# Kernel optimization log

Hardware: AMD Instinct MI355X
Metric: run time of the kernel (lower is better)

The kernel has to match this reference:

```python
import jax, jax.numpy as jnp
from jax import lax
import numpy as np

BETA = 0.9
SLOPE = 25.0  # snntorch fast_sigmoid default slope

@jax.custom_vjp
def spike_fn(mem_shift):
    # Heaviside forward, fast-sigmoid surrogate backward
    return (mem_shift > 0).astype(mem_shift.dtype)

def _spike_fwd(mem_shift):
    return spike_fn(mem_shift), mem_shift

def _spike_bwd(mem_shift, g):
    return (g / (SLOPE * jnp.abs(mem_shift) + 1.0) ** 2,)

spike_fn.defvjp(_spike_fwd, _spike_bwd)

def lif_step(inp, mem, thr):
    # snntorch Leaky, reset_mechanism='subtract': reset computed from PREVIOUS mem, detached
    reset = lax.stop_gradient((mem - thr > 0).astype(mem.dtype))
    mem_new = BETA * mem + inp - reset * thr  # thr keeps grad through reset term
    spk = spike_fn(mem_new - thr)
    return spk, mem_new

def _linear_init(key, out_f, in_f):
    k1, k2 = jax.random.split(key)
    bound = 1.0 / np.sqrt(in_f)
    W = jax.random.uniform(k1, (out_f, in_f), jnp.float32, -bound, bound)
    b = jax.random.uniform(k2, (out_f,), jnp.float32, -bound, bound)
    return W, b

def setup_inputs() -> dict:
    key = jax.random.key(0)
    ks = jax.random.split(key, 6)
    B, T = 2048, 112
    x = jax.random.normal(ks[0], (B, T, 4), jnp.float32)
    W1, b1 = _linear_init(ks[1], 1300, 4)
    W2, b2 = _linear_init(ks[2], 340, 1300)
    W3, b3 = _linear_init(ks[3], 1400, 340)
    W4, b4 = _linear_init(ks[4], 4, 1400)
    return {
        'x': x,
        'W1': W1, 'b1': b1, 'bias1': jnp.zeros((1300,), jnp.float32),
        'W2': W2, 'b2': b2, 'bias2': jnp.zeros((340,), jnp.float32),
        'W3': W3, 'b3': b3, 'bias3': jnp.zeros((1400,), jnp.float32),
        'W4': W4, 'b4': b4, 'bias4': jnp.zeros((4,), jnp.float32),
        'thr4': jnp.asarray(0.5, jnp.float32),
    }

def reference(x, W1, b1, bias1, W2, b2, bias2, W3, b3, bias3, W4, b4, bias4, thr4):
    B, T, _ = x.shape
    one = jnp.asarray(1.0, x.dtype)

    def step(carry, xt):
        m1, m2, m3, m4 = carry
        xt = xt / 50.0 + 0.001
        s1, m1 = lif_step(xt @ W1.T + b1 + bias1, m1, one)
        s2, m2 = lif_step(s1 @ W2.T + b2 + bias2, m2, one)
        s3, m3 = lif_step(s2 @ W3.T + b3 + bias3, m3, one)
        s4, m4 = lif_step(s3 @ W4.T + b4 + bias4, m4, thr4)
        return (m1, m2, m3, m4), s4

    init = tuple(jnp.zeros((B, d), x.dtype) for d in (1300, 340, 1400, 4))
    _, spk4 = lax.scan(step, init, jnp.swapaxes(x, 0, 1))  # [T,B,4]
    spk4_stack = jnp.swapaxes(spk4, 0, 1)  # [B,T,4]
    spike_counts = spk4_stack.sum(axis=1)  # [B,4]
    return spike_counts, spk4_stack
```

## Files before the change

### kernel.cpp

```cpp
#include <hip/hip_runtime.h>

#define B_ROWS  2048
#define T_STEPS 112
#define N1 1300
#define N2 340
#define N3 1400

#define R1 192
#define R2 64
#define R3 192

#define OFF_W2T 0
#define OFF_W3T 442000
#define OFF_W4T 918000
#define OFF_BS1 923600
#define OFF_BS2 924900
#define OFF_BS3 925240
#define OFF_BS4 926640
#define WS_FLOATS 926644

__global__ __launch_bounds__(256) void snn_prep(
    const float* __restrict__ W2, const float* __restrict__ W3, const float* __restrict__ W4,
    const float* __restrict__ b1, const float* __restrict__ bias1,
    const float* __restrict__ b2, const float* __restrict__ bias2,
    const float* __restrict__ b3, const float* __restrict__ bias3,
    const float* __restrict__ b4, const float* __restrict__ bias4,
    float* __restrict__ ws)
{
    for (int idx = blockIdx.x * blockDim.x + threadIdx.x; idx < WS_FLOATS;
         idx += gridDim.x * blockDim.x) {
        float v;
        if (idx < OFF_W3T) {
            int j = idx; int i = j / N2, k = j % N2;
            v = W2[k * N1 + i];
        } else if (idx < OFF_W4T) {
            int j = idx - OFF_W3T; int i = j / N3, k = j % N3;
            v = W3[k * N2 + i];
        } else if (idx < OFF_BS1) {
            int j = idx - OFF_W4T; int i = j / 4, k = j % 4;
            v = W4[k * N3 + i];
        } else if (idx < OFF_BS2) { int j = idx - OFF_BS1; v = b1[j] + bias1[j]; }
        else if (idx < OFF_BS3)   { int j = idx - OFF_BS2; v = b2[j] + bias2[j]; }
        else if (idx < OFF_BS4)   { int j = idx - OFF_BS3; v = b3[j] + bias3[j]; }
        else                      { int j = idx - OFF_BS4; v = b4[j] + bias4[j]; }
        ws[idx] = v;
    }
}

__device__ __forceinline__ float2 pk_add(float2 a, float2 b) {
    float2 d;
    asm("v_pk_add_f32 %0, %1, %2" : "=v"(d) : "v"(a), "v"(b));
    return d;
}
__device__ __forceinline__ void pk_acc4(float4& acc, const float4 r) {
    float2 lo = pk_add(make_float2(acc.x, acc.y), make_float2(r.x, r.y));
    float2 hi = pk_add(make_float2(acc.z, acc.w), make_float2(r.z, r.w));
    acc.x = lo.x; acc.y = lo.y; acc.z = hi.x; acc.w = hi.y;
}

__global__ __launch_bounds__(512, 4) void snn_main(
    const float* __restrict__ x,
    const float* __restrict__ W1,
    const float* __restrict__ ws,
    const float* __restrict__ thr4p,
    float* __restrict__ out)
{
    const int b    = blockIdx.x;
    const int tid  = threadIdx.x;
    const int wave = tid >> 6;
    const int lane = tid & 63;

    const float* __restrict__ W2T = ws + OFF_W2T;
    const float* __restrict__ W3T = ws + OFF_W3T;
    const float* __restrict__ W4T = ws + OFF_W4T;
    const float* __restrict__ bs1 = ws + OFF_BS1;
    const float* __restrict__ bs2 = ws + OFF_BS2;
    const float* __restrict__ bs3 = ws + OFF_BS3;
    const float* __restrict__ bs4 = ws + OFF_BS4;

    __shared__ __align__(16) float pw2[8][340];
    __shared__ __align__(16) float pw3[8][1400];
    __shared__ __align__(16) unsigned short lst1[8 * R1];
    __shared__ __align__(16) unsigned short lst2[8 * R2];
    __shared__ __align__(16) unsigned short lst3[8 * R3];
    __shared__ float h4part[8][4];

    const int c1b = (wave < 5) ? 3 * wave : 15 + 2 * (wave - 5);
    const int n1  = (wave < 5) ? 3 : 2;

    float mem1[3] = {0.f,0.f,0.f};
    float mem2 = 0.f;
    float mem3[3] = {0.f,0.f,0.f};
    float mem4 = 0.f;
    float cnt  = 0.f;
    const float thr4 = thr4p[0];

    const float4* __restrict__ xv4 = (const float4*)x;
    const float4* __restrict__ W1v = (const float4*)W1;

    int  k1v[3]; bool val1[3]; float bsv1[3];
    #pragma unroll
    for (int u = 0; u < 3; ++u) {
        k1v[u] = (c1b + u) * 64 + lane;
        val1[u] = (u < n1) && (k1v[u] < N1);
        bsv1[u] = val1[u] ? bs1[k1v[u]] : 0.f;
    }
    const bool  act2 = (tid < N2);
    const float bs2v = act2 ? bs2[tid] : 0.f;
    const bool  act3hi = (tid < 376);
    float bs3v[3];
    bs3v[0] = bs3[tid];
    bs3v[1] = bs3[tid + 512];
    bs3v[2] = act3hi ? bs3[tid + 1024] : 0.f;
    const float bs4v = bs4[lane & 3];

    const int so2 = (lane < 21) ? 4 * lane : 80;
    const int so3 = (lane < 30) ? 4 * lane : 116;

    for (int t = 0; t < T_STEPS; ++t) {
        float4 xv = xv4[b * T_STEPS + t];
        const float x0 = xv.x / 50.0f + 0.001f;
        const float x1 = xv.y / 50.0f + 0.001f;
        const float x2 = xv.z / 50.0f + 0.001f;
        const float x3 = xv.w / 50.0f + 0.001f;

        unsigned cnt1w = 0;
        #pragma unroll
        for (int u = 0; u < 3; ++u) {
            if (u < n1) {
                float h = 0.f;
                if (val1[u]) {
                    float4 wv = W1v[k1v[u]];
                    h = bsv1[u] + wv.x * x0 + wv.y * x1 + wv.z * x2 + wv.w * x3;
                }
                float m = mem1[u];
                const float r = (m > 1.0f) ? 1.0f : 0.0f;
                m = 0.9f * m + h - r;
                mem1[u] = m;
                const bool sp = val1[u] && (m > 1.0f);
                const unsigned long long bal = __ballot(sp);
                if (sp) {
                    const int pos = (int)cnt1w + (int)__popcll(bal & ((1ull << lane) - 1ull));
                    lst1[wave * R1 + pos] = (unsigned short)k1v[u];
                }
                cnt1w += (unsigned)__popcll(bal);
            }
        }

        {
            float4 accA = {0.f,0.f,0.f,0.f};
            float4 accB = {0.f,0.f,0.f,0.f};
            const unsigned short* L = lst1 + wave * R1;
            const float* baseA = W2T + 4 * lane;
            const float* baseB = W2T + 256 + so2;
            const int n = (int)cnt1w;
            int j = 0;
            if (n >= 4) {
                ushort4 i0 = *(const ushort4*)(L);
                int o0 = (int)i0.x * N2, o1 = (int)i0.y * N2;
                int o2 = (int)i0.z * N2, o3 = (int)i0.w * N2;
                float4 rA0 = *(const float4*)(baseA + o0);
                float4 rA1 = *(const float4*)(baseA + o1);
                float4 rA2 = *(const float4*)(baseA + o2);
                float4 rA3 = *(const float4*)(baseA + o3);
                float4 rB0 = *(const float4*)(baseB + o0);
                float4 rB1 = *(const float4*)(baseB + o1);
                float4 rB2 = *(const float4*)(baseB + o2);
                float4 rB3 = *(const float4*)(baseB + o3);
                for (j = 4; j + 4 <= n; j += 4) {
                    ushort4 i1 = *(const ushort4*)(L + j);
                    const int p0 = (int)i1.x * N2, p1 = (int)i1.y * N2;
                    const int p2 = (int)i1.z * N2, p3 = (int)i1.w * N2;
                    float4 sA0 = *(const float4*)(baseA + p0);
                    float4 sA1 = *(const float4*)(baseA + p1);
                    float4 sA2 = *(const float4*)(baseA + p2);
                    float4 sA3 = *(const float4*)(baseA + p3);
                    float4 sB0 = *(const float4*)(baseB + p0);
                    float4 sB1 = *(const float4*)(baseB + p1);
                    float4 sB2 = *(const float4*)(baseB + p2);
                    float4 sB3 = *(const float4*)(baseB + p3);
                    pk_acc4(accA, rA0); pk_acc4(accB, rB0);
                    pk_acc4(accA, rA1); pk_acc4(accB, rB1);
                    pk_acc4(accA, rA2); pk_acc4(accB, rB2);
                    pk_acc4(accA, rA3); pk_acc4(accB, rB3);
                    rA0 = sA0; rA1 = sA1; rA2 = sA2; rA3 = sA3;
                    rB0 = sB0; rB1 = sB1; rB2 = sB2; rB3 = sB3;
                }
                pk_acc4(accA, rA0); pk_acc4(accB, rB0);
                pk_acc4(accA, rA1); pk_acc4(accB, rB1);
                pk_acc4(accA, rA2); pk_acc4(accB, rB2);
                pk_acc4(accA, rA3); pk_acc4(accB, rB3);
            }
            for (; j < n; ++j) {
                const int o = (int)L[j] * N2;
                float4 rA = *(const float4*)(baseA + o);
                float4 rB = *(const float4*)(baseB + o);
                pk_acc4(accA, rA); pk_acc4(accB, rB);
            }
            *(float4*)&pw2[wave][4 * lane] = accA;
            if (lane < 21) *(float4*)&pw2[wave][256 + 4 * lane] = accB;
        }
        __syncthreads();

        if (wave == 7 && t > 0) {
            float h4 = bs4v;
            #pragma unroll
            for (int p = 0; p < 8; ++p) h4 += h4part[p][lane & 3];
            float m4 = mem4;
            const float r4 = (m4 > thr4) ? thr4 : 0.f;
            m4 = 0.9f * m4 + h4 - r4;
            mem4 = m4;
            const float s4 = (m4 > thr4) ? 1.f : 0.f;
            if (lane < 4) {
                out[8192 + (b * T_STEPS + (t - 1)) * 4 + lane] = s4;
                cnt += s4;
            }
        }

        unsigned cnt2w = 0;
        {
            float h0 = 0.f;
            if (act2) {
                h0 = pw2[0][tid] + pw2[1][tid] + pw2[2][tid] + pw2[3][tid]
                   + pw2[4][tid] + pw2[5][tid] + pw2[6][tid] + pw2[7][tid] + bs2v;
            }
            float m = mem2;
            const float r = (m > 1.0f) ? 1.0f : 0.0f;
            m = 0.9f * m + h0 - r;
            mem2 = m;
            const bool sp0 = act2 && (m > 1.0f);
            const unsigned long long bal0 = __ballot(sp0);
            if (sp0) {
                const int pos = (int)__popcll(bal0 & ((1ull << lane) - 1ull));
                lst2[wave * R2 + pos] = (unsigned short)tid;
            }
            cnt2w = (unsigned)__popcll(bal0);
        }

        {
            float4 acc3[6];
            #pragma unroll
            for (int c = 0; c < 6; ++c) acc3[c] = (float4){0.f,0.f,0.f,0.f};
            const unsigned short* L = lst2 + wave * R2;
            int j = 0;
            for (; j + 2 <= (int)cnt2w; j += 2) {
                ushort2 ii = *(const ushort2*)(L + j);
                const float* ra = W3T + (int)ii.x * N3;
                const float* rb = W3T + (int)ii.y * N3;
                float4 a0 = *(const float4*)(ra + 4*lane);
                float4 a1 = *(const float4*)(ra + 256 + 4*lane);
                float4 a2 = *(const float4*)(ra + 512 + 4*lane);
                float4 a3 = *(const float4*)(ra + 768 + 4*lane);
                float4 a4 = *(const float4*)(ra + 1024 + 4*lane);
                float4 a5 = *(const float4*)(ra + 1280 + so3);
                float4 b0 = *(const float4*)(rb + 4*lane);
                float4 b1_ = *(const float4*)(rb + 256 + 4*lane);
                float4 b2_ = *(const float4*)(rb + 512 + 4*lane);
                float4 b3_ = *(const float4*)(rb + 768 + 4*lane);
                float4 b4_ = *(const float4*)(rb + 1024 + 4*lane);
                float4 b5_ = *(const float4*)(rb + 1280 + so3);
                pk_acc4(acc3[0], a0); pk_acc4(acc3[1], a1); pk_acc4(acc3[2], a2);
                pk_acc4(acc3[3], a3); pk_acc4(acc3[4], a4); pk_acc4(acc3[5], a5);
                pk_acc4(acc3[0], b0); pk_acc4(acc3[1], b1_); pk_acc4(acc3[2], b2_);
                pk_acc4(acc3[3], b3_); pk_acc4(acc3[4], b4_); pk_acc4(acc3[5], b5_);
            }
            for (; j < (int)cnt2w; ++j) {
                const float* ra = W3T + (int)L[j] * N3;
                float4 a0 = *(const float4*)(ra + 4*lane);
                float4 a1 = *(const float4*)(ra + 256 + 4*lane);
                float4 a2 = *(const float4*)(ra + 512 + 4*lane);
                float4 a3 = *(const float4*)(ra + 768 + 4*lane);
                float4 a4 = *(const float4*)(ra + 1024 + 4*lane);
                float4 a5 = *(const float4*)(ra + 1280 + so3);
                pk_acc4(acc3[0], a0); pk_acc4(acc3[1], a1); pk_acc4(acc3[2], a2);
                pk_acc4(acc3[3], a3); pk_acc4(acc3[4], a4); pk_acc4(acc3[5], a5);
            }
            #pragma unroll
            for (int c = 0; c < 5; ++c)
                *(float4*)&pw3[wave][c * 256 + 4 * lane] = acc3[c];
            if (lane < 30) *(float4*)&pw3[wave][1280 + 4 * lane] = acc3[5];
        }
        __syncthreads();

        {
            unsigned cnt3w = 0;
            #pragma unroll
            for (int k = 0; k < 3; ++k) {
                const bool valid = (k < 2) || act3hi;
                const int n = tid + 512 * k;
                float h = 0.f;
                if (valid) {
                    h = pw3[0][n] + pw3[1][n] + pw3[2][n] + pw3[3][n]
                      + pw3[4][n] + pw3[5][n] + pw3[6][n] + pw3[7][n] + bs3v[k];
                }
                float m = mem3[k];
                const float r = (m > 1.0f) ? 1.0f : 0.0f;
                m = 0.9f * m + h - r;
                mem3[k] = m;
                const bool sp = valid && (m > 1.0f);
                const unsigned long long bal = __ballot(sp);
                if (sp) {
                    const int pos = (int)cnt3w + (int)__popcll(bal & ((1ull << lane) - 1ull));
                    lst3[wave * R3 + pos] = (unsigned short)n;
                }
                cnt3w += (unsigned)__popcll(bal);
            }
            float h4p = 0.f;
            const unsigned short* L = lst3 + wave * R3;
            const int o4 = lane & 3;
            int j = 0;
            for (; j + 4 <= (int)cnt3w; j += 4) {
                ushort4 ii = *(const ushort4*)(L + j);
                float t0 = W4T[4 * (int)ii.x + o4];
                float t1 = W4T[4 * (int)ii.y + o4];
                float t2 = W4T[4 * (int)ii.z + o4];
                float t3 = W4T[4 * (int)ii.w + o4];
                h4p += t0; h4p += t1; h4p += t2; h4p += t3;
            }
            for (; j < (int)cnt3w; ++j) h4p += W4T[4 * (int)L[j] + o4];
            if (lane < 4) h4part[wave][lane] = h4p;
        }
    }

    __syncthreads();
    if (wave == 7) {
        float h4 = bs4v;
        #pragma unroll
        for (int p = 0; p < 8; ++p) h4 += h4part[p][lane & 3];
        float m4 = mem4;
        const float r4 = (m4 > thr4) ? thr4 : 0.f;
        m4 = 0.9f * m4 + h4 - r4;
        const float s4 = (m4 > thr4) ? 1.f : 0.f;
        if (lane < 4) {
            out[8192 + (b * T_STEPS + (T_STEPS - 1)) * 4 + lane] = s4;
            cnt += s4;
            out[b * 4 + lane] = cnt;
        }
    }
}

extern "C" void kernel_launch(void* const* d_in, const int* in_sizes, int n_in,
                              void* d_out, int out_size, void* d_ws, size_t ws_size,
                              hipStream_t stream)
{
    const float* x     = (const float*)d_in[0];
    const float* W1    = (const float*)d_in[1];
    const float* b1    = (const float*)d_in[2];
    const float* bias1 = (const float*)d_in[3];
    const float* W2    = (const float*)d_in[4];
    const float* b2    = (const float*)d_in[5];
    const float* bias2 = (const float*)d_in[6];
    const float* W3    = (const float*)d_in[7];
    const float* b3    = (const float*)d_in[8];
    const float* bias3 = (const float*)d_in[9];
    const float* W4    = (const float*)d_in[10];
    const float* b4    = (const float*)d_in[11];
    const float* bias4 = (const float*)d_in[12];
    const float* thr4  = (const float*)d_in[13];
    float* out = (float*)d_out;
    float* ws  = (float*)d_ws;

    hipLaunchKernelGGL(snn_prep, dim3(1024), dim3(256), 0, stream,
                       W2, W3, W4, b1, bias1, b2, bias2, b3, bias3, b4, bias4, ws);
    hipLaunchKernelGGL(snn_main, dim3(B_ROWS), dim3(512), 0, stream,
                       x, W1, ws, thr4, out);
}
```

Measured before the change: 2.350 ms.

## Shrink SNN block to two waves with more neurons per thread

Reduces the per-batch-row block from 8 waves to 2. Each thread now owns 11 layer-1 neurons, 3 layer-2 neurons and 11 layer-3 neurons, and the spike-list capacities are enlarged to match. The aim is to cut cross-wave partial-sum reductions and barrier cost, since shared-memory reductions drop from 8 partials to 2. The trade-off is fewer threads to hide latency, longer serial gather loops per wave over the sparse weight rows, and much higher register pressure from the per-thread membrane arrays.

```diff
diff --git a/kernel.cpp b/kernel.cpp
--- a/kernel.cpp
+++ b/kernel.cpp
@@ -6,9 +6,9 @@
 #define N2 340
 #define N3 1400
 
-#define R1 192
-#define R2 64
-#define R3 192
+#define R1 704
+#define R2 192
+#define R3 704
 
 #define OFF_W2T 0
 #define OFF_W3T 442000
@@ -58,7 +58,7 @@
     acc.x = lo.x; acc.y = lo.y; acc.z = hi.x; acc.w = hi.y;
 }
 
-__global__ __launch_bounds__(512, 4) void snn_main(
+__global__ __launch_bounds__(128, 4) void snn_main(
     const float* __restrict__ x,
     const float* __restrict__ W1,
     const float* __restrict__ ws,
@@ -78,19 +78,19 @@
     const float* __restrict__ bs3 = ws + OFF_BS3;
     const float* __restrict__ bs4 = ws + OFF_BS4;
 
-    __shared__ __align__(16) float pw2[8][340];
-    __shared__ __align__(16) float pw3[8][1400];
-    __shared__ __align__(16) unsigned short lst1[8 * R1];
-    __shared__ __align__(16) unsigned short lst2[8 * R2];
-    __shared__ __align__(16) unsigned short lst3[8 * R3];
-    __shared__ float h4part[8][4];
-
-    const int c1b = (wave < 5) ? 3 * wave : 15 + 2 * (wave - 5);
-    const int n1  = (wave < 5) ? 3 : 2;
-
-    float mem1[3] = {0.f,0.f,0.f};
-    float mem2 = 0.f;
-    float mem3[3] = {0.f,0.f,0.f};
+    __shared__ __align__(16) float pw2[2][340];
+    __shared__ __align__(16) float pw3[2][1400];
+    __shared__ __align__(16) unsigned short lst1[2 * R1];
+    __shared__ __align__(16) unsigned short lst2[2 * R2];
+    __shared__ __align__(16) unsigned short lst3[2 * R3];
+    __shared__ float h4part[2][4];
+
+    const int c1b = wave * 11;
+    const int n1  = 11 - wave;
+
+    float mem1[11] = {0.f,0.f,0.f,0.f,0.f,0.f,0.f,0.f,0.f,0.f,0.f};
+    float mem2[3]  = {0.f,0.f,0.f};
+    float mem3[11] = {0.f,0.f,0.f,0.f,0.f,0.f,0.f,0.f,0.f,0.f,0.f};
     float mem4 = 0.f;
     float cnt  = 0.f;
     const float thr4 = thr4p[0];
@@ -98,20 +98,24 @@
     const float4* __restrict__ xv4 = (const float4*)x;
     const float4* __restrict__ W1v = (const float4*)W1;
 
-    int  k1v[3]; bool val1[3]; float bsv1[3];
+    float bsv1[11];
     #pragma unroll
-    for (int u = 0; u < 3; ++u) {
-        k1v[u] = (c1b + u) * 64 + lane;
-        val1[u] = (u < n1) && (k1v[u] < N1);
-        bsv1[u] = val1[u] ? bs1[k1v[u]] : 0.f;
-    }
-    const bool  act2 = (tid < N2);
-    const float bs2v = act2 ? bs2[tid] : 0.f;
-    const bool  act3hi = (tid < 376);
-    float bs3v[3];
-    bs3v[0] = bs3[tid];
-    bs3v[1] = bs3[tid + 512];
-    bs3v[2] = act3hi ? bs3[tid + 1024] : 0.f;
+    for (int u = 0; u < 11; ++u) {
+        const int k1 = (c1b + u) * 64 + lane;
+        bsv1[u] = ((u < n1) && (k1 < N1)) ? bs1[k1] : 0.f;
+    }
+    float bs2v[3];
+    #pragma unroll
+    for (int k = 0; k < 3; ++k) {
+        const bool valid = (k < 2) || (tid < 84);
+        bs2v[k] = valid ? bs2[tid + 128 * k] : 0.f;
+    }
+    float bs3v[11];
+    #pragma unroll
+    for (int k = 0; k < 11; ++k) {
+        const bool valid = (k < 10) || (tid < 120);
+        bs3v[k] = valid ? bs3[tid + 128 * k] : 0.f;
+    }
     const float bs4v = bs4[lane & 3];
 
     const int so2 = (lane < 21) ? 4 * lane : 80;
@@ -126,22 +130,24 @@
 
         unsigned cnt1w = 0;
         #pragma unroll
-        for (int u = 0; u < 3; ++u) {
+        for (int u = 0; u < 11; ++u) {
             if (u < n1) {
+                const int k1 = (c1b + u) * 64 + lane;
+                const bool valid = (k1 < N1);
                 float h = 0.f;
-                if (val1[u]) {
-                    float4 wv = W1v[k1v[u]];
+                if (valid) {
+                    float4 wv = W1v[k1];
                     h = bsv1[u] + wv.x * x0 + wv.y * x1 + wv.z * x2 + wv.w * x3;
                 }
                 float m = mem1[u];
                 const float r = (m > 1.0f) ? 1.0f : 0.0f;
                 m = 0.9f * m + h - r;
                 mem1[u] = m;
-                const bool sp = val1[u] && (m > 1.0f);
+                const bool sp = valid && (m > 1.0f);
                 const unsigned long long bal = __ballot(sp);
                 if (sp) {
                     const int pos = (int)cnt1w + (int)__popcll(bal & ((1ull << lane) - 1ull));
-                    lst1[wave * R1 + pos] = (unsigned short)k1v[u];
+                    lst1[wave * R1 + pos] = (unsigned short)k1;
                 }
                 cnt1w += (unsigned)__popcll(bal);
             }
@@ -202,10 +208,9 @@
         }
         __syncthreads();
 
-        if (wave == 7 && t > 0) {
-            float h4 = bs4v;
-            #pragma unroll
-            for (int p = 0; p < 8; ++p) h4 += h4part[p][lane & 3];
+        if (wave == 1 && t > 0) {
+            float h4 = bs4v + h4part[0][lane & 3];
+            h4 += h4part[1][lane & 3];
             float m4 = mem4;
             const float r4 = (m4 > thr4) ? thr4 : 0.f;
             m4 = 0.9f * m4 + h4 - r4;
@@ -218,23 +223,23 @@
         }
 
         unsigned cnt2w = 0;
-        {
-            float h0 = 0.f;
-            if (act2) {
-                h0 = pw2[0][tid] + pw2[1][tid] + pw2[2][tid] + pw2[3][tid]
-                   + pw2[4][tid] + pw2[5][tid] + pw2[6][tid] + pw2[7][tid] + bs2v;
-            }
-            float m = mem2;
+        #pragma unroll
+        for (int k = 0; k < 3; ++k) {
+            const bool valid = (k < 2) || (tid < 84);
+            const int n = tid + 128 * k;
+            float h = 0.f;
+            if (valid) h = pw2[0][n] + pw2[1][n] + bs2v[k];
+            float m = mem2[k];
             const float r = (m > 1.0f) ? 1.0f : 0.0f;
-            m = 0.9f * m + h0 - r;
-            mem2 = m;
-            const bool sp0 = act2 && (m > 1.0f);
-            const unsigned long long bal0 = __ballot(sp0);
-            if (sp0) {
-                const int pos = (int)__popcll(bal0 & ((1ull << lane) - 1ull));
-                lst2[wave * R2 + pos] = (unsigned short)tid;
-            }
-            cnt2w = (unsigned)__popcll(bal0);
+            m = 0.9f * m + h - r;
+            mem2[k] = m;
+            const bool sp = valid && (m > 1.0f);
+            const unsigned long long bal = __ballot(sp);
+            if (sp) {
+                const int pos = (int)cnt2w + (int)__popcll(bal & ((1ull << lane) - 1ull));
+                lst2[wave * R2 + pos] = (unsigned short)n;
+            }
+            cnt2w += (unsigned)__popcll(bal);
         }
 
         {
@@ -285,14 +290,11 @@
         {
             unsigned cnt3w = 0;
             #pragma unroll
-            for (int k = 0; k < 3; ++k) {
-                const bool valid = (k < 2) || act3hi;
-                const int n = tid + 512 * k;
+            for (int k = 0; k < 11; ++k) {
+                const bool valid = (k < 10) || (tid < 120);
+                const int n = tid + 128 * k;
                 float h = 0.f;
-                if (valid) {
-                    h = pw3[0][n] + pw3[1][n] + pw3[2][n] + pw3[3][n]
-                      + pw3[4][n] + pw3[5][n] + pw3[6][n] + pw3[7][n] + bs3v[k];
-                }
+                if (valid) h = pw3[0][n] + pw3[1][n] + bs3v[k];
                 float m = mem3[k];
                 const float r = (m > 1.0f) ? 1.0f : 0.0f;
                 m = 0.9f * m + h - r;
@@ -323,10 +325,9 @@
     }
 
     __syncthreads();
-    if (wave == 7) {
-        float h4 = bs4v;
-        #pragma unroll
-        for (int p = 0; p < 8; ++p) h4 += h4part[p][lane & 3];
+    if (wave == 1) {
+        float h4 = bs4v + h4part[0][lane & 3];
+        h4 += h4part[1][lane & 3];
         float m4 = mem4;
         const float r4 = (m4 > thr4) ? thr4 : 0.f;
         m4 = 0.9f * m4 + h4 - r4;
@@ -362,6 +363,6 @@
 
     hipLaunchKernelGGL(snn_prep, dim3(1024), dim3(256), 0, stream,
                        W2, W3, W4, b1, bias1, b2, bias2, b3, bias3, b4, bias4, ws);
-    hipLaunchKernelGGL(snn_main, dim3(B_ROWS), dim3(512), 0, stream,
+    hipLaunchKernelGGL(snn_main, dim3(B_ROWS), dim3(128), 0, stream,
                        x, W1, ws, thr4, out);
 }
```

New measurement: 2.708 ms. +15.2%, slower.
